# Kernel optimization log

Measured on AMD Instinct MI355X. Metric: run time of the kernel, lower is better.

Reference implementation:

```python
import jax, jax.numpy as jnp
import numpy as np

D_MODEL = 1024
D_HIDDEN = 4096
NUM_EXPERTS = 8
K_ACTIVE = 2


def setup_inputs() -> dict:
    key = jax.random.key(0)
    ks = jax.random.split(key, 8)
    x = jax.random.normal(ks[0], (1, 2048, D_MODEL), dtype=jnp.float32)
    gate_w = jax.random.normal(ks[1], (D_MODEL, NUM_EXPERTS), dtype=jnp.float32) * 0.02
    gate_b = jnp.zeros((NUM_EXPERTS,), dtype=jnp.float32)
    w1 = jax.random.normal(ks[2], (NUM_EXPERTS, D_MODEL, D_HIDDEN), dtype=jnp.float32) * 0.02
    b1 = jnp.zeros((NUM_EXPERTS, D_HIDDEN), dtype=jnp.float32)
    w2 = jax.random.normal(ks[3], (NUM_EXPERTS, D_HIDDEN, D_MODEL), dtype=jnp.float32) * 0.02
    b2 = jnp.zeros((NUM_EXPERTS, D_MODEL), dtype=jnp.float32)
    return {"x": x, "gate_w": gate_w, "gate_b": gate_b,
            "w1": w1, "b1": b1, "w2": w2, "b2": b2}


def reference(x, gate_w, gate_b, w1, b1, w2, b2):
    B, S, D = x.shape
    xf = x.reshape(-1, D)                                    # [T, D]
    logits = xf @ gate_w + gate_b                            # [T, E]
    top_w, top_idx = jax.lax.top_k(logits, K_ACTIVE)         # [T, K]
    top_w = jax.nn.softmax(top_w, axis=-1)                   # softmax over selected experts
    # combine-weight per expert: sum over k slots of one-hot(idx) * weight -> [T, E]
    gates = jnp.sum(jax.nn.one_hot(top_idx, NUM_EXPERTS, dtype=xf.dtype) * top_w[..., None], axis=1)
    # expert FFN applied per expert (dropout is identity in eval): gelu is exact (erf), matching torch nn.GELU default
    h = jax.nn.gelu(jnp.einsum('td,edh->teh', xf, w1) + b1[None], approximate=False)  # [T, E, H]
    y = jnp.einsum('teh,ehd->ted', h, w2) + b2[None]         # [T, E, D]
    out = jnp.einsum('ted,te->td', y, gates)                 # weighted combine of selected experts
    return out.reshape(B, S, D)
```

## Files before the change

### kernel.cpp

```cpp
#include <hip/hip_runtime.h>
#include <stdint.h>

typedef unsigned short u16;
typedef __attribute__((ext_vector_type(8))) short s16x8;
typedef __attribute__((ext_vector_type(8))) u16  u16x8;
typedef __attribute__((ext_vector_type(4))) u16  u16x4;
typedef __attribute__((ext_vector_type(4))) float f32x4;

#define T_TOKENS 2048
#define DM 1024
#define DH 4096
#define NE 8
#define BM 128
#define BN 128
#define BK 64
#define MAXSLOTS (T_TOKENS*2 + NE*BM)
#define ROWBLK (MAXSLOTS/BM)

__device__ __forceinline__ u16 f2bf(float f) {
    union { float ff; uint32_t u; } v; v.ff = f;
    uint32_t r = v.u + 0x7fffu + ((v.u >> 16) & 1u);
    return (u16)(r >> 16);
}

#define GLOAD_LDS16(gsrc, ldst) \
    __builtin_amdgcn_global_load_lds((const __attribute__((address_space(1))) uint32_t*)(gsrc), \
                                     (__attribute__((address_space(3))) uint32_t*)(ldst), 16, 0, 0)

#define WAIT_VM8() asm volatile("s_waitcnt vmcnt(8)" ::: "memory")
#define WAIT_VM0() asm volatile("s_waitcnt vmcnt(0)" ::: "memory")

__global__ void k_convert(const float* __restrict__ x, u16* __restrict__ xbf,
                          int* __restrict__ ctrl) {
    int i = blockIdx.x * blockDim.x + threadIdx.x;
    const f32x4* xv = (const f32x4*)x;
    f32x4 a = xv[2*i], b = xv[2*i+1];
    u16x8 o;
    o[0]=f2bf(a[0]); o[1]=f2bf(a[1]); o[2]=f2bf(a[2]); o[3]=f2bf(a[3]);
    o[4]=f2bf(b[0]); o[5]=f2bf(b[1]); o[6]=f2bf(b[2]); o[7]=f2bf(b[3]);
    ((u16x8*)xbf)[i] = o;
    if (blockIdx.x == 0 && threadIdx.x < 32) ctrl[threadIdx.x] = 0;
}

__global__ void __launch_bounds__(256) k_transpose(const float* __restrict__ src,
                                                   u16* __restrict__ dst,
                                                   int K, int N) {
    __shared__ float tile[64][65];
    const int e = blockIdx.z;
    const int n0 = blockIdx.x * 64, k0 = blockIdx.y * 64;
    const float* s = src + (size_t)e * K * N;
    u16* d = dst + (size_t)e * K * N;
    const int tx = threadIdx.x & 15, ty = threadIdx.x >> 4;
    #pragma unroll
    for (int j = 0; j < 4; ++j) {
        int r = ty * 4 + j;
        f32x4 v = *(const f32x4*)(s + (size_t)(k0 + r) * N + n0 + tx * 4);
        tile[r][tx*4+0] = v[0]; tile[r][tx*4+1] = v[1];
        tile[r][tx*4+2] = v[2]; tile[r][tx*4+3] = v[3];
    }
    __syncthreads();
    #pragma unroll
    for (int j = 0; j < 4; ++j) {
        int n = ty * 4 + j;
        u16x4 w;
        #pragma unroll
        for (int c = 0; c < 4; ++c) w[c] = f2bf(tile[tx*4+c][n]);
        *(u16x4*)(d + (size_t)(n0 + n) * K + k0 + tx * 4) = w;
    }
}

__global__ void __launch_bounds__(64) k_gate(const float* __restrict__ x,
                                             const float* __restrict__ gw,
                                             const float* __restrict__ gb,
                                             int* __restrict__ cnt,
                                             int* __restrict__ tt_idx,
                                             float* __restrict__ tt_w) {
    const int t = blockIdx.x;
    const int lane = threadIdx.x;
    float acc[NE] = {0.f,0.f,0.f,0.f,0.f,0.f,0.f,0.f};
    const float* xr = x + (size_t)t * DM;
    #pragma unroll
    for (int c = 0; c < DM/64; ++c) {
        float xv = xr[lane + 64*c];
        const float* g = gw + (size_t)(lane + 64*c) * NE;
        #pragma unroll
        for (int e = 0; e < NE; ++e) acc[e] += xv * g[e];
    }
    #pragma unroll
    for (int e = 0; e < NE; ++e) {
        #pragma unroll
        for (int off = 32; off >= 1; off >>= 1)
            acc[e] += __shfl_xor(acc[e], off, 64);
    }
    if (lane == 0) {
        float l[NE];
        #pragma unroll
        for (int e = 0; e < NE; ++e) l[e] = acc[e] + gb[e];
        int i0 = 0;
        #pragma unroll
        for (int e = 1; e < NE; ++e) if (l[e] > l[i0]) i0 = e;
        int i1 = (i0 == 0) ? 1 : 0;
        #pragma unroll
        for (int e = 0; e < NE; ++e) if (e != i0 && l[e] > l[i1]) i1 = e;
        float m  = l[i0];
        float w0 = expf(l[i0] - m), w1 = expf(l[i1] - m);
        float s = w0 + w1; w0 /= s; w1 /= s;
        tt_idx[t*2] = i0; tt_idx[t*2+1] = i1;
        tt_w[t*2] = w0;  tt_w[t*2+1] = w1;
        atomicAdd(&cnt[i0], 1); atomicAdd(&cnt[i1], 1);
    }
}

__global__ void k_offsets(const int* __restrict__ cnt, int* __restrict__ fill,
                          int* __restrict__ off) {
    if (threadIdx.x == 0 && blockIdx.x == 0) {
        int a = 0;
        for (int e = 0; e < NE; ++e) {
            off[e] = a;
            a += (cnt[e] + BM - 1) / BM * BM;
            fill[e] = 0;
        }
        off[NE] = a;
    }
}

__global__ void k_scatter(const int* __restrict__ tt_idx, const float* __restrict__ tt_w,
                          const int* __restrict__ off, int* __restrict__ fill,
                          int* __restrict__ slot_token, float* __restrict__ slot_gate,
                          int* __restrict__ tok_slot) {
    int t = blockIdx.x * blockDim.x + threadIdx.x;
    if (t >= T_TOKENS) return;
    #pragma unroll
    for (int k = 0; k < 2; ++k) {
        int e = tt_idx[t*2+k];
        int pos = off[e] + atomicAdd(&fill[e], 1);
        slot_token[pos] = t;
        slot_gate[pos]  = tt_w[t*2+k];
        tok_slot[t*2+k] = pos;
    }
}

__device__ __forceinline__ void mma64(const u16* As, const u16* Bs, int lane,
                                      int wr, int wc, f32x4 acc[4][4]) {
    #pragma unroll
    for (int ko = 0; ko < 2; ++ko) {
        s16x8 af[4], bfr[4];
        #pragma unroll
        for (int m = 0; m < 4; ++m) {
            int row = wr*64 + m*16 + (lane & 15);
            int sl = (ko*4 + (lane >> 4)) ^ (row & 7);
            af[m] = *(const s16x8*)&As[row*BK + sl*8];
        }
        #pragma unroll
        for (int n = 0; n < 4; ++n) {
            int col = wc*64 + n*16 + (lane & 15);
            int sl = (ko*4 + (lane >> 4)) ^ (col & 7);
            bfr[n] = *(const s16x8*)&Bs[col*BK + sl*8];
        }
        #pragma unroll
        for (int m = 0; m < 4; ++m)
            #pragma unroll
            for (int n = 0; n < 4; ++n)
                acc[m][n] = __builtin_amdgcn_mfma_f32_16x16x32_bf16(af[m], bfr[n], acc[m][n], 0, 0, 0);
    }
}


__global__ void __launch_bounds__(256) k_ffn1_b16(
    const u16* __restrict__ xbf, const u16* __restrict__ w1t,
    const float* __restrict__ b1, const int* __restrict__ slot_token,
    const int* __restrict__ off, u16* __restrict__ h)
{
    __shared__ u16 As[2][BM*BK];
    __shared__ u16 Bs[2][BN*BK];
    const int rb = blockIdx.y, cb = blockIdx.x;
    const int total = off[NE];
    const int r0 = rb * BM;
    if (r0 >= total) return;
    int e = 0;
    while (e < NE-1 && off[e+1] <= r0) e++;
    const u16* Bsrc = w1t + (size_t)e * DM * DH;
    const float* be = b1 + (size_t)e * DH;

    const int tid = threadIdx.x;
    const int lane = tid & 63, wid = tid >> 6;
    const int wr = wid >> 1, wc = wid & 1;

    const u16* gA[4]; const u16* gB[4];
    #pragma unroll
    for (int i = 0; i < 4; ++i) {
        int row = wid*32 + i*8 + (lane >> 3);
        int g = (lane & 7) ^ (row & 7);
        int tok = slot_token[r0 + row];
        gA[i] = xbf + (size_t)tok * DM + g*8;
        gB[i] = Bsrc + (size_t)(cb*BN + row) * DM + g*8;
    }

    f32x4 acc[4][4];
    #pragma unroll
    for (int m = 0; m < 4; ++m)
        #pragma unroll
        for (int n = 0; n < 4; ++n) acc[m][n] = (f32x4){0.f,0.f,0.f,0.f};

    #define STAGE1(buf, kt) do {                                              \
        _Pragma("unroll")                                                     \
        for (int i = 0; i < 4; ++i) {                                         \
            GLOAD_LDS16(gA[i] + (kt)*BK, &As[buf][(wid*32 + i*8)*BK]);        \
            GLOAD_LDS16(gB[i] + (kt)*BK, &Bs[buf][(wid*32 + i*8)*BK]);        \
        }                                                                     \
    } while (0)

    const int NT = DM / BK;
    STAGE1(0, 0);
    STAGE1(1, 1);
    #pragma unroll 1
    for (int kt = 0; kt < NT; ++kt) {
        if (kt + 1 < NT) WAIT_VM8(); else WAIT_VM0();
        __builtin_amdgcn_s_barrier();
        __builtin_amdgcn_s_setprio(1);
        mma64(As[kt & 1], Bs[kt & 1], lane, wr, wc, acc);
        __builtin_amdgcn_s_setprio(0);
        __builtin_amdgcn_s_barrier();
        if (kt + 2 < NT) STAGE1(kt & 1, kt + 2);
    }
    #undef STAGE1

    #pragma unroll
    for (int n = 0; n < 4; ++n) {
        int col = cb*BN + wc*64 + n*16 + (lane & 15);
        float bb = be[col];
        #pragma unroll
        for (int m = 0; m < 4; ++m) {
            int rbase = r0 + wr*64 + m*16 + (lane >> 4)*4;
            #pragma unroll
            for (int i = 0; i < 4; ++i) {
                float v = acc[m][n][i] + bb;
                float gv = 0.5f * v * (1.0f + erff(v * 0.70710678118654752f));
                h[(size_t)(rbase + i)*DH + col] = f2bf(gv);
            }
        }
    }
}

__global__ void __launch_bounds__(256) k_ffn2_b16(
    const u16* __restrict__ h, const u16* __restrict__ w2t,
    const float* __restrict__ b2, const int* __restrict__ slot_token,
    const float* __restrict__ slot_gate, const int* __restrict__ off,
    float* __restrict__ out, float* __restrict__ partial, int ktiles)
{
    __shared__ u16 As[2][BM*BK];
    __shared__ u16 Bs[2][BN*BK];
    const int rb = blockIdx.y, cb = blockIdx.x, kz = blockIdx.z;
    const int total = off[NE];
    const int r0 = rb * BM;
    if (r0 >= total) return;
    int e = 0;
    while (e < NE-1 && off[e+1] <= r0) e++;
    const u16* Bsrc = w2t + (size_t)e * DH * DM;
    const float* be = b2 + (size_t)e * DM;
    const int kt0 = kz * ktiles;

    const int tid = threadIdx.x;
    const int lane = tid & 63, wid = tid >> 6;
    const int wr = wid >> 1, wc = wid & 1;

    const u16* gA[4]; const u16* gB[4];
    #pragma unroll
    for (int i = 0; i < 4; ++i) {
        int row = wid*32 + i*8 + (lane >> 3);
        int g = (lane & 7) ^ (row & 7);
        gA[i] = h + (size_t)(r0 + row) * DH + (size_t)kt0*BK + g*8;
        gB[i] = Bsrc + (size_t)(cb*BN + row) * DH + (size_t)kt0*BK + g*8;
    }

    f32x4 acc[4][4];
    #pragma unroll
    for (int m = 0; m < 4; ++m)
        #pragma unroll
        for (int n = 0; n < 4; ++n) acc[m][n] = (f32x4){0.f,0.f,0.f,0.f};

    #define STAGE2(buf, kt) do {                                              \
        _Pragma("unroll")                                                     \
        for (int i = 0; i < 4; ++i) {                                         \
            GLOAD_LDS16(gA[i] + (kt)*BK, &As[buf][(wid*32 + i*8)*BK]);        \
            GLOAD_LDS16(gB[i] + (kt)*BK, &Bs[buf][(wid*32 + i*8)*BK]);        \
        }                                                                     \
    } while (0)

    const int NT = ktiles;
    STAGE2(0, 0);
    STAGE2(1, 1);
    #pragma unroll 1
    for (int kt = 0; kt < NT; ++kt) {
        if (kt + 1 < NT) WAIT_VM8(); else WAIT_VM0();
        __builtin_amdgcn_s_barrier();
        __builtin_amdgcn_s_setprio(1);
        mma64(As[kt & 1], Bs[kt & 1], lane, wr, wc, acc);
        __builtin_amdgcn_s_setprio(0);
        __builtin_amdgcn_s_barrier();
        if (kt + 2 < NT) STAGE2(kt & 1, kt + 2);
    }
    #undef STAGE2

    if (partial) {
        #pragma unroll
        for (int m = 0; m < 4; ++m) {
            #pragma unroll
            for (int i = 0; i < 4; ++i) {
                int s = r0 + wr*64 + m*16 + (lane >> 4)*4 + i;
                float* prow = partial + (size_t)s * DM + cb*BN + wc*64;
                #pragma unroll
                for (int n = 0; n < 4; ++n)
                    atomicAdd(prow + n*16 + (lane & 15), acc[m][n][i]);
            }
        }
    } else {
        float bb[4];
        #pragma unroll
        for (int n = 0; n < 4; ++n) bb[n] = be[cb*BN + wc*64 + n*16 + (lane & 15)];
        #pragma unroll
        for (int m = 0; m < 4; ++m) {
            #pragma unroll
            for (int i = 0; i < 4; ++i) {
                int s = r0 + wr*64 + m*16 + (lane >> 4)*4 + i;
                int tok = slot_token[s];
                float g = slot_gate[s];
                if (g != 0.0f) {
                    float* orow = out + (size_t)tok * DM + cb*BN + wc*64;
                    #pragma unroll
                    for (int n = 0; n < 4; ++n)
                        atomicAdd(orow + n*16 + (lane & 15), g * (acc[m][n][i] + bb[n]));
                }
            }
        }
    }
}

__global__ void __launch_bounds__(256) k_combine(
    const float* __restrict__ partial, const float* __restrict__ b2,
    const int* __restrict__ tok_slot, const int* __restrict__ tt_idx,
    const float* __restrict__ tt_w, float* __restrict__ out)
{
    const int t = blockIdx.x;
    const int d = threadIdx.x * 4;
    const int s0 = tok_slot[t*2], s1 = tok_slot[t*2+1];
    const int e0 = tt_idx[t*2],  e1 = tt_idx[t*2+1];
    const float g0 = tt_w[t*2],  g1 = tt_w[t*2+1];
    f32x4 p0 = *(const f32x4*)(partial + (size_t)s0 * DM + d);
    f32x4 p1 = *(const f32x4*)(partial + (size_t)s1 * DM + d);
    f32x4 bb0 = *(const f32x4*)(b2 + (size_t)e0 * DM + d);
    f32x4 bb1 = *(const f32x4*)(b2 + (size_t)e1 * DM + d);
    f32x4 o;
    #pragma unroll
    for (int c = 0; c < 4; ++c) o[c] = g0 * (p0[c] + bb0[c]) + g1 * (p1[c] + bb1[c]);
    *(f32x4*)(out + (size_t)t * DM + d) = o;
}


__global__ void __launch_bounds__(256) k_ffn1_f32(
    const u16* __restrict__ xbf, const float* __restrict__ w1,
    const float* __restrict__ b1, const int* __restrict__ slot_token,
    const int* __restrict__ off, u16* __restrict__ h)
{
    __shared__ u16 As[BM*BK];
    __shared__ u16 Bs[BN*BK];
    const int rb = blockIdx.y, cb = blockIdx.x;
    const int total = off[NE];
    const int r0 = rb * BM;
    if (r0 >= total) return;
    int e = 0;
    while (e < NE-1 && off[e+1] <= r0) e++;
    const float* Bsrc = w1 + (size_t)e * DM * DH;
    const float* be   = b1 + (size_t)e * DH;

    const int tid = threadIdx.x;
    const int lane = tid & 63, wid = tid >> 6;
    const int wr = wid >> 1, wc = wid & 1;

    const u16* gA[4];
    #pragma unroll
    for (int i = 0; i < 4; ++i) {
        int row = wid*32 + i*8 + (lane >> 3);
        int g = (lane & 7) ^ (row & 7);
        int tok = slot_token[r0 + row];
        gA[i] = xbf + (size_t)tok * DM + g*8;
    }
    const int tc = tid & 31, tr = tid >> 5;
    const float* gB = Bsrc + (size_t)(tr*8) * DH + cb*BN + tc*4;

    f32x4 acc[4][4];
    #pragma unroll
    for (int m = 0; m < 4; ++m)
        #pragma unroll
        for (int n = 0; n < 4; ++n) acc[m][n] = (f32x4){0.f,0.f,0.f,0.f};

    for (int kt = 0; kt < DM/BK; ++kt) {
        #pragma unroll
        for (int i = 0; i < 4; ++i)
            GLOAD_LDS16(gA[i] + kt*BK, &As[(wid*32 + i*8)*BK]);
        f32x4 bv[8];
        #pragma unroll
        for (int j = 0; j < 8; ++j)
            bv[j] = *(const f32x4*)(gB + (size_t)(kt*BK + j) * DH);
        #pragma unroll
        for (int c = 0; c < 4; ++c) {
            int n = tc*4 + c;
            int sl = tr ^ (n & 7);
            s16x8 pk;
            #pragma unroll
            for (int j = 0; j < 8; ++j) pk[j] = (short)f2bf(bv[j][c]);
            *(s16x8*)&Bs[n*BK + sl*8] = pk;
        }
        __syncthreads();
        mma64(As, Bs, lane, wr, wc, acc);
        __syncthreads();
    }
    #pragma unroll
    for (int n = 0; n < 4; ++n) {
        int col = cb*BN + wc*64 + n*16 + (lane & 15);
        float bb = be[col];
        #pragma unroll
        for (int m = 0; m < 4; ++m) {
            int rbase = r0 + wr*64 + m*16 + (lane >> 4)*4;
            #pragma unroll
            for (int i = 0; i < 4; ++i) {
                float v = acc[m][n][i] + bb;
                float gv = 0.5f * v * (1.0f + erff(v * 0.70710678118654752f));
                h[(size_t)(rbase + i)*DH + col] = f2bf(gv);
            }
        }
    }
}

__global__ void __launch_bounds__(256) k_ffn2_f32(
    const u16* __restrict__ h, const float* __restrict__ w2,
    const float* __restrict__ b2, const int* __restrict__ slot_token,
    const float* __restrict__ slot_gate, const int* __restrict__ off,
    float* __restrict__ out)
{
    __shared__ u16 As[BM*BK];
    __shared__ u16 Bs[BN*BK];
    const int rb = blockIdx.y, cb = blockIdx.x;
    const int total = off[NE];
    const int r0 = rb * BM;
    if (r0 >= total) return;
    int e = 0;
    while (e < NE-1 && off[e+1] <= r0) e++;
    const float* Bsrc = w2 + (size_t)e * DH * DM;
    const float* be   = b2 + (size_t)e * DM;

    const int tid = threadIdx.x;
    const int lane = tid & 63, wid = tid >> 6;
    const int wr = wid >> 1, wc = wid & 1;

    const u16* gA[4];
    #pragma unroll
    for (int i = 0; i < 4; ++i) {
        int row = wid*32 + i*8 + (lane >> 3);
        int g = (lane & 7) ^ (row & 7);
        gA[i] = h + (size_t)(r0 + row) * DH + g*8;
    }
    const int tc = tid & 31, tr = tid >> 5;
    const float* gB = Bsrc + (size_t)(tr*8) * DM + cb*BN + tc*4;

    f32x4 acc[4][4];
    #pragma unroll
    for (int m = 0; m < 4; ++m)
        #pragma unroll
        for (int n = 0; n < 4; ++n) acc[m][n] = (f32x4){0.f,0.f,0.f,0.f};

    for (int kt = 0; kt < DH/BK; ++kt) {
        #pragma unroll
        for (int i = 0; i < 4; ++i)
            GLOAD_LDS16(gA[i] + kt*BK, &As[(wid*32 + i*8)*BK]);
        f32x4 bv[8];
        #pragma unroll
        for (int j = 0; j < 8; ++j)
            bv[j] = *(const f32x4*)(gB + (size_t)(kt*BK + j) * DM);
        #pragma unroll
        for (int c = 0; c < 4; ++c) {
            int n = tc*4 + c;
            int sl = tr ^ (n & 7);
            s16x8 pk;
            #pragma unroll
            for (int j = 0; j < 8; ++j) pk[j] = (short)f2bf(bv[j][c]);
            *(s16x8*)&Bs[n*BK + sl*8] = pk;
        }
        __syncthreads();
        mma64(As, Bs, lane, wr, wc, acc);
        __syncthreads();
    }
    float bb[4];
    #pragma unroll
    for (int n = 0; n < 4; ++n) bb[n] = be[cb*BN + wc*64 + n*16 + (lane & 15)];
    #pragma unroll
    for (int m = 0; m < 4; ++m) {
        #pragma unroll
        for (int i = 0; i < 4; ++i) {
            int s = r0 + wr*64 + m*16 + (lane >> 4)*4 + i;
            int tok = slot_token[s];
            float g = slot_gate[s];
            if (g != 0.0f) {
                float* orow = out + (size_t)tok * DM + cb*BN + wc*64;
                #pragma unroll
                for (int n = 0; n < 4; ++n)
                    atomicAdd(orow + n*16 + (lane & 15), g * (acc[m][n][i] + bb[n]));
            }
        }
    }
}

extern "C" void kernel_launch(void* const* d_in, const int* in_sizes, int n_in,
                              void* d_out, int out_size, void* d_ws, size_t ws_size,
                              hipStream_t stream)
{
    (void)in_sizes; (void)n_in; (void)out_size;
    const float* x  = (const float*)d_in[0];
    const float* gw = (const float*)d_in[1];
    const float* gb = (const float*)d_in[2];
    const float* w1 = (const float*)d_in[3];
    const float* b1 = (const float*)d_in[4];
    const float* w2 = (const float*)d_in[5];
    const float* b2 = (const float*)d_in[6];
    float* out = (float*)d_out;
    char* ws = (char*)d_ws;

    const size_t OFF_XBF = 0;
    const size_t OFF_H   = 4194304;
    const size_t OFF_WT  = OFF_H + (size_t)MAXSLOTS * DH * 2;
    const size_t OFF_ST  = OFF_WT + (size_t)NE * DM * DH * 2;
    const size_t OFF_SG  = OFF_ST + MAXSLOTS * 4;
    const size_t OFF_TI  = OFF_SG + MAXSLOTS * 4;
    const size_t OFF_TW  = OFF_TI + T_TOKENS * 2 * 4;
    const size_t OFF_TS  = OFF_TW + T_TOKENS * 2 * 4;
    const size_t OFF_CT  = OFF_TS + T_TOKENS * 2 * 4;
    const size_t NEED_B16 = OFF_CT + 128;
    const size_t OFF_PT  = (NEED_B16 + 255) & ~(size_t)255;
    const size_t NEED_SPLIT = OFF_PT + (size_t)MAXSLOTS * DM * 4;

    if (ws_size >= NEED_B16) {
        u16*   xbf        = (u16*)(ws + OFF_XBF);
        u16*   h          = (u16*)(ws + OFF_H);
        u16*   wt         = (u16*)(ws + OFF_WT);
        int*   slot_token = (int*)(ws + OFF_ST);
        float* slot_gate  = (float*)(ws + OFF_SG);
        int*   tt_idx     = (int*)(ws + OFF_TI);
        float* tt_w       = (float*)(ws + OFF_TW);
        int*   tok_slot   = (int*)(ws + OFF_TS);
        int*   ctrl       = (int*)(ws + OFF_CT);
        float* partial    = (float*)(ws + OFF_PT);
        int* cnt = ctrl; int* fill = ctrl + 8; int* offs = ctrl + 16;
        const int use_split = (ws_size >= NEED_SPLIT);

        hipMemsetAsync(slot_token, 0, 2 * MAXSLOTS * 4, stream);
        if (use_split)
            hipMemsetAsync(partial, 0, (size_t)MAXSLOTS * DM * 4, stream);
        else
            hipMemsetAsync(out, 0, (size_t)T_TOKENS * DM * sizeof(float), stream);

        k_convert<<<(T_TOKENS*DM/8 + 255)/256, 256, 0, stream>>>(x, xbf, ctrl);
        k_gate<<<T_TOKENS, 64, 0, stream>>>(x, gw, gb, cnt, tt_idx, tt_w);
        k_offsets<<<1, 64, 0, stream>>>(cnt, fill, offs);
        k_scatter<<<(T_TOKENS + 255)/256, 256, 0, stream>>>(tt_idx, tt_w, offs, fill,
                                                            slot_token, slot_gate, tok_slot);

        k_transpose<<<dim3(DH/64, DM/64, NE), 256, 0, stream>>>(w1, wt, DM, DH);
        k_ffn1_b16<<<dim3(DH/BN, ROWBLK), 256, 0, stream>>>(xbf, wt, b1, slot_token, offs, h);
        k_transpose<<<dim3(DM/64, DH/64, NE), 256, 0, stream>>>(w2, wt, DH, DM);

        if (use_split) {
            k_ffn2_b16<<<dim3(DM/BN, ROWBLK, 2), 256, 0, stream>>>(
                h, wt, b2, slot_token, slot_gate, offs, out, partial, DH/BK/2);
            k_combine<<<T_TOKENS, 256, 0, stream>>>(partial, b2, tok_slot, tt_idx, tt_w, out);
        } else {
            k_ffn2_b16<<<dim3(DM/BN, ROWBLK, 1), 256, 0, stream>>>(
                h, wt, b2, slot_token, slot_gate, offs, out, (float*)nullptr, DH/BK);
        }
    } else {
        u16*   xbf        = (u16*)(ws);
        u16*   h          = (u16*)(ws + 4194304);
        int*   slot_token = (int*)(ws + 46137344);
        float* slot_gate  = (float*)(ws + 46157824);
        int*   tt_idx     = (int*)(ws + 46178304);
        float* tt_w       = (float*)(ws + 46194688);
        int*   tok_slot   = (int*)(ws + 46211072);
        int*   ctrl       = (int*)(ws + 46227456);
        int* cnt = ctrl; int* fill = ctrl + 8; int* offs = ctrl + 16;

        hipMemsetAsync(slot_token, 0, 2 * MAXSLOTS * 4, stream);
        hipMemsetAsync(out, 0, (size_t)T_TOKENS * DM * sizeof(float), stream);

        k_convert<<<(T_TOKENS*DM/8 + 255)/256, 256, 0, stream>>>(x, xbf, ctrl);
        k_gate<<<T_TOKENS, 64, 0, stream>>>(x, gw, gb, cnt, tt_idx, tt_w);
        k_offsets<<<1, 64, 0, stream>>>(cnt, fill, offs);
        k_scatter<<<(T_TOKENS + 255)/256, 256, 0, stream>>>(tt_idx, tt_w, offs, fill,
                                                            slot_token, slot_gate, tok_slot);
        k_ffn1_f32<<<dim3(DH/BN, ROWBLK), 256, 0, stream>>>(xbf, w1, b1, slot_token, offs, h);
        k_ffn2_f32<<<dim3(DM/BN, ROWBLK), 256, 0, stream>>>(h, w2, b2, slot_token, slot_gate, offs, out);
    }
}
```

Baseline: 341.3 us.

## Use 256x256 tiles for FFN1, pad experts to 256, drop FFN2 split-K

Replaces the 128x128 first-layer expert GEMM with a 256x256-tile kernel using 512 threads and 8x4 MFMA accumulators per wave, and pads each expert's slot range to 256 rows. The larger tile raises data reuse per LDS load and halves the number of row blocks. The split-K second GEMM with its partial buffer and combine pass is removed, so FFN2 always atomically adds gated results straight into the output. A half-width weight transpose path is added for smaller workspaces. The extra padding rows add wasted compute, and the larger tile raises register and LDS pressure.

```diff
diff --git a/kernel.cpp b/kernel.cpp
--- a/kernel.cpp
+++ b/kernel.cpp
@@ -11,9 +11,13 @@
 #define DM 1024
 #define DH 4096
 #define NE 8
+#define BK 64
+#define PAD2 256
+#define MAXS2 (T_TOKENS*2 + NE*PAD2)
+#define RB1 (MAXS2/256)
+#define RB2 (MAXS2/128)
 #define BM 128
 #define BN 128
-#define BK 64
 #define MAXSLOTS (T_TOKENS*2 + NE*BM)
 #define ROWBLK (MAXSLOTS/BM)
 
@@ -44,12 +48,12 @@
 
 __global__ void __launch_bounds__(256) k_transpose(const float* __restrict__ src,
                                                    u16* __restrict__ dst,
-                                                   int K, int N) {
+                                                   int K, int N, int nw0, int NW) {
     __shared__ float tile[64][65];
     const int e = blockIdx.z;
-    const int n0 = blockIdx.x * 64, k0 = blockIdx.y * 64;
+    const int n0 = nw0 + blockIdx.x * 64, k0 = blockIdx.y * 64;
     const float* s = src + (size_t)e * K * N;
-    u16* d = dst + (size_t)e * K * N;
+    u16* d = dst + (size_t)e * K * NW;
     const int tx = threadIdx.x & 15, ty = threadIdx.x >> 4;
     #pragma unroll
     for (int j = 0; j < 4; ++j) {
@@ -65,7 +69,7 @@
         u16x4 w;
         #pragma unroll
         for (int c = 0; c < 4; ++c) w[c] = f2bf(tile[tx*4+c][n]);
-        *(u16x4*)(d + (size_t)(n0 + n) * K + k0 + tx * 4) = w;
+        *(u16x4*)(d + (size_t)(n0 - nw0 + n) * K + k0 + tx * 4) = w;
     }
 }
 
@@ -112,12 +116,12 @@
 }
 
 __global__ void k_offsets(const int* __restrict__ cnt, int* __restrict__ fill,
-                          int* __restrict__ off) {
+                          int* __restrict__ off, int pad) {
     if (threadIdx.x == 0 && blockIdx.x == 0) {
         int a = 0;
         for (int e = 0; e < NE; ++e) {
             off[e] = a;
-            a += (cnt[e] + BM - 1) / BM * BM;
+            a += (cnt[e] + pad - 1) / pad * pad;
             fill[e] = 0;
         }
         off[NE] = a;
@@ -126,8 +130,7 @@
 
 __global__ void k_scatter(const int* __restrict__ tt_idx, const float* __restrict__ tt_w,
                           const int* __restrict__ off, int* __restrict__ fill,
-                          int* __restrict__ slot_token, float* __restrict__ slot_gate,
-                          int* __restrict__ tok_slot) {
+                          int* __restrict__ slot_token, float* __restrict__ slot_gate) {
     int t = blockIdx.x * blockDim.x + threadIdx.x;
     if (t >= T_TOKENS) return;
     #pragma unroll
@@ -136,7 +139,6 @@
         int pos = off[e] + atomicAdd(&fill[e], 1);
         slot_token[pos] = t;
         slot_gate[pos]  = tt_w[t*2+k];
-        tok_slot[t*2+k] = pos;
     }
 }
 
@@ -165,11 +167,113 @@
     }
 }
 
-
-__global__ void __launch_bounds__(256) k_ffn1_b16(
-    const u16* __restrict__ xbf, const u16* __restrict__ w1t,
+__device__ __forceinline__ void mma256(const u16* As, const u16* Bs, int lane,
+                                       int wr, int wc, f32x4 acc[8][4]) {
+    #pragma unroll
+    for (int ko = 0; ko < 2; ++ko) {
+        s16x8 af[8], bfr[4];
+        #pragma unroll
+        for (int m = 0; m < 8; ++m) {
+            int row = wr*128 + m*16 + (lane & 15);
+            int sl = (ko*4 + (lane >> 4)) ^ (row & 7);
+            af[m] = *(const s16x8*)&As[row*BK + sl*8];
+        }
+        #pragma unroll
+        for (int n = 0; n < 4; ++n) {
+            int col = wc*64 + n*16 + (lane & 15);
+            int sl = (ko*4 + (lane >> 4)) ^ (col & 7);
+            bfr[n] = *(const s16x8*)&Bs[col*BK + sl*8];
+        }
+        #pragma unroll
+        for (int m = 0; m < 8; ++m)
+            #pragma unroll
+            for (int n = 0; n < 4; ++n)
+                acc[m][n] = __builtin_amdgcn_mfma_f32_16x16x32_bf16(af[m], bfr[n], acc[m][n], 0, 0, 0);
+    }
+}
+
+__global__ void __launch_bounds__(512, 2) k_ffn1_256(
+    const u16* __restrict__ xbf, const u16* __restrict__ wt,
     const float* __restrict__ b1, const int* __restrict__ slot_token,
-    const int* __restrict__ off, u16* __restrict__ h)
+    const int* __restrict__ off, u16* __restrict__ h, int cb0, int NW)
+{
+    __shared__ u16 As[2][256*BK];
+    __shared__ u16 Bs[2][256*BK];
+    const int rb = blockIdx.y, cbl = blockIdx.x;
+    const int total = off[NE];
+    const int r0 = rb * 256;
+    if (r0 >= total) return;
+    int e = 0;
+    while (e < NE-1 && off[e+1] <= r0) e++;
+    const u16* Bsrc = wt + (size_t)e * DM * NW;
+    const float* be = b1 + (size_t)e * DH;
+    const int colbase = (cb0 + cbl) * 256;
+
+    const int tid = threadIdx.x;
+    const int lane = tid & 63, wid = tid >> 6;
+    const int wr = wid >> 2, wc = wid & 3;
+
+    const u16* gA[4]; const u16* gB[4];
+    #pragma unroll
+    for (int i = 0; i < 4; ++i) {
+        int row = wid*32 + i*8 + (lane >> 3);
+        int g = (lane & 7) ^ (row & 7);
+        int tok = slot_token[r0 + row];
+        gA[i] = xbf + (size_t)tok * DM + g*8;
+        gB[i] = Bsrc + (size_t)(cbl*256 + row) * DM + g*8;
+    }
+
+    f32x4 acc[8][4];
+    #pragma unroll
+    for (int m = 0; m < 8; ++m)
+        #pragma unroll
+        for (int n = 0; n < 4; ++n) acc[m][n] = (f32x4){0.f,0.f,0.f,0.f};
+
+    #define STG1(buf, kt) do {                                                \
+        _Pragma("unroll")                                                     \
+        for (int i = 0; i < 4; ++i) {                                         \
+            GLOAD_LDS16(gA[i] + (kt)*BK, &As[buf][(wid*32 + i*8)*BK]);        \
+            GLOAD_LDS16(gB[i] + (kt)*BK, &Bs[buf][(wid*32 + i*8)*BK]);        \
+        }                                                                     \
+    } while (0)
+
+    const int NT = DM / BK;
+    STG1(0, 0);
+    STG1(1, 1);
+    #pragma unroll 1
+    for (int kt = 0; kt < NT; ++kt) {
+        if (kt + 1 < NT) WAIT_VM8(); else WAIT_VM0();
+        __builtin_amdgcn_s_barrier();
+        __builtin_amdgcn_s_setprio(1);
+        mma256(As[kt & 1], Bs[kt & 1], lane, wr, wc, acc);
+        __builtin_amdgcn_s_setprio(0);
+        __builtin_amdgcn_s_barrier();
+        if (kt + 2 < NT) STG1(kt & 1, kt + 2);
+    }
+    #undef STG1
+
+    #pragma unroll
+    for (int n = 0; n < 4; ++n) {
+        int col = colbase + wc*64 + n*16 + (lane & 15);
+        float bb = be[col];
+        #pragma unroll
+        for (int m = 0; m < 8; ++m) {
+            int rbase = r0 + wr*128 + m*16 + (lane >> 4)*4;
+            #pragma unroll
+            for (int i = 0; i < 4; ++i) {
+                float v = acc[m][n][i] + bb;
+                float gv = 0.5f * v * (1.0f + erff(v * 0.70710678118654752f));
+                h[(size_t)(rbase + i)*DH + col] = f2bf(gv);
+            }
+        }
+    }
+}
+
+__global__ void __launch_bounds__(256) k_ffn2_b16(
+    const u16* __restrict__ h, const u16* __restrict__ w2t,
+    const float* __restrict__ b2, const int* __restrict__ slot_token,
+    const float* __restrict__ slot_gate, const int* __restrict__ off,
+    float* __restrict__ out)
 {
     __shared__ u16 As[2][BM*BK];
     __shared__ u16 Bs[2][BN*BK];
@@ -179,8 +283,8 @@
     if (r0 >= total) return;
     int e = 0;
     while (e < NE-1 && off[e+1] <= r0) e++;
-    const u16* Bsrc = w1t + (size_t)e * DM * DH;
-    const float* be = b1 + (size_t)e * DH;
+    const u16* Bsrc = w2t + (size_t)e * DH * DM;
+    const float* be = b2 + (size_t)e * DM;
 
     const int tid = threadIdx.x;
     const int lane = tid & 63, wid = tid >> 6;
@@ -191,9 +295,8 @@
     for (int i = 0; i < 4; ++i) {
         int row = wid*32 + i*8 + (lane >> 3);
         int g = (lane & 7) ^ (row & 7);
-        int tok = slot_token[r0 + row];
-        gA[i] = xbf + (size_t)tok * DM + g*8;
-        gB[i] = Bsrc + (size_t)(cb*BN + row) * DM + g*8;
+        gA[i] = h + (size_t)(r0 + row) * DH + g*8;
+        gB[i] = Bsrc + (size_t)(cb*BN + row) * DH + g*8;
     }
 
     f32x4 acc[4][4];
@@ -202,7 +305,7 @@
         #pragma unroll
         for (int n = 0; n < 4; ++n) acc[m][n] = (f32x4){0.f,0.f,0.f,0.f};
 
-    #define STAGE1(buf, kt) do {                                              \
+    #define STG2(buf, kt) do {                                                \
         _Pragma("unroll")                                                     \
         for (int i = 0; i < 4; ++i) {                                         \
             GLOAD_LDS16(gA[i] + (kt)*BK, &As[buf][(wid*32 + i*8)*BK]);        \
@@ -210,9 +313,9 @@
         }                                                                     \
     } while (0)
 
-    const int NT = DM / BK;
-    STAGE1(0, 0);
-    STAGE1(1, 1);
+    const int NT = DH / BK;
+    STG2(0, 0);
+    STG2(1, 1);
     #pragma unroll 1
     for (int kt = 0; kt < NT; ++kt) {
         if (kt + 1 < NT) WAIT_VM8(); else WAIT_VM0();
@@ -221,139 +324,28 @@
         mma64(As[kt & 1], Bs[kt & 1], lane, wr, wc, acc);
         __builtin_amdgcn_s_setprio(0);
         __builtin_amdgcn_s_barrier();
-        if (kt + 2 < NT) STAGE1(kt & 1, kt + 2);
-    }
-    #undef STAGE1
-
-    #pragma unroll
-    for (int n = 0; n < 4; ++n) {
-        int col = cb*BN + wc*64 + n*16 + (lane & 15);
-        float bb = be[col];
-        #pragma unroll
-        for (int m = 0; m < 4; ++m) {
-            int rbase = r0 + wr*64 + m*16 + (lane >> 4)*4;
-            #pragma unroll
-            for (int i = 0; i < 4; ++i) {
-                float v = acc[m][n][i] + bb;
-                float gv = 0.5f * v * (1.0f + erff(v * 0.70710678118654752f));
-                h[(size_t)(rbase + i)*DH + col] = f2bf(gv);
-            }
-        }
-    }
-}
-
-__global__ void __launch_bounds__(256) k_ffn2_b16(
-    const u16* __restrict__ h, const u16* __restrict__ w2t,
-    const float* __restrict__ b2, const int* __restrict__ slot_token,
-    const float* __restrict__ slot_gate, const int* __restrict__ off,
-    float* __restrict__ out, float* __restrict__ partial, int ktiles)
-{
-    __shared__ u16 As[2][BM*BK];
-    __shared__ u16 Bs[2][BN*BK];
-    const int rb = blockIdx.y, cb = blockIdx.x, kz = blockIdx.z;
-    const int total = off[NE];
-    const int r0 = rb * BM;
-    if (r0 >= total) return;
-    int e = 0;
-    while (e < NE-1 && off[e+1] <= r0) e++;
-    const u16* Bsrc = w2t + (size_t)e * DH * DM;
-    const float* be = b2 + (size_t)e * DM;
-    const int kt0 = kz * ktiles;
-
-    const int tid = threadIdx.x;
-    const int lane = tid & 63, wid = tid >> 6;
-    const int wr = wid >> 1, wc = wid & 1;
-
-    const u16* gA[4]; const u16* gB[4];
-    #pragma unroll
-    for (int i = 0; i < 4; ++i) {
-        int row = wid*32 + i*8 + (lane >> 3);
-        int g = (lane & 7) ^ (row & 7);
-        gA[i] = h + (size_t)(r0 + row) * DH + (size_t)kt0*BK + g*8;
-        gB[i] = Bsrc + (size_t)(cb*BN + row) * DH + (size_t)kt0*BK + g*8;
-    }
-
-    f32x4 acc[4][4];
-    #pragma unroll
-    for (int m = 0; m < 4; ++m)
-        #pragma unroll
-        for (int n = 0; n < 4; ++n) acc[m][n] = (f32x4){0.f,0.f,0.f,0.f};
-
-    #define STAGE2(buf, kt) do {                                              \
-        _Pragma("unroll")                                                     \
-        for (int i = 0; i < 4; ++i) {                                         \
-            GLOAD_LDS16(gA[i] + (kt)*BK, &As[buf][(wid*32 + i*8)*BK]);        \
-            GLOAD_LDS16(gB[i] + (kt)*BK, &Bs[buf][(wid*32 + i*8)*BK]);        \
-        }                                                                     \
-    } while (0)
-
-    const int NT = ktiles;
-    STAGE2(0, 0);
-    STAGE2(1, 1);
-    #pragma unroll 1
-    for (int kt = 0; kt < NT; ++kt) {
-        if (kt + 1 < NT) WAIT_VM8(); else WAIT_VM0();
-        __builtin_amdgcn_s_barrier();
-        __builtin_amdgcn_s_setprio(1);
-        mma64(As[kt & 1], Bs[kt & 1], lane, wr, wc, acc);
-        __builtin_amdgcn_s_setprio(0);
-        __builtin_amdgcn_s_barrier();
-        if (kt + 2 < NT) STAGE2(kt & 1, kt + 2);
-    }
-    #undef STAGE2
-
-    if (partial) {
-        #pragma unroll
-        for (int m = 0; m < 4; ++m) {
-            #pragma unroll
-            for (int i = 0; i < 4; ++i) {
-                int s = r0 + wr*64 + m*16 + (lane >> 4)*4 + i;
-                float* prow = partial + (size_t)s * DM + cb*BN + wc*64;
+        if (kt + 2 < NT) STG2(kt & 1, kt + 2);
+    }
+    #undef STG2
+
+    float bb[4];
+    #pragma unroll
+    for (int n = 0; n < 4; ++n) bb[n] = be[cb*BN + wc*64 + n*16 + (lane & 15)];
+    #pragma unroll
+    for (int m = 0; m < 4; ++m) {
+        #pragma unroll
+        for (int i = 0; i < 4; ++i) {
+            int s = r0 + wr*64 + m*16 + (lane >> 4)*4 + i;
+            int tok = slot_token[s];
+            float g = slot_gate[s];
+            if (g != 0.0f) {
+                float* orow = out + (size_t)tok * DM + cb*BN + wc*64;
                 #pragma unroll
                 for (int n = 0; n < 4; ++n)
-                    atomicAdd(prow + n*16 + (lane & 15), acc[m][n][i]);
+                    atomicAdd(orow + n*16 + (lane & 15), g * (acc[m][n][i] + bb[n]));
             }
         }
-    } else {
-        float bb[4];
-        #pragma unroll
-        for (int n = 0; n < 4; ++n) bb[n] = be[cb*BN + wc*64 + n*16 + (lane & 15)];
-        #pragma unroll
-        for (int m = 0; m < 4; ++m) {
-            #pragma unroll
-            for (int i = 0; i < 4; ++i) {
-                int s = r0 + wr*64 + m*16 + (lane >> 4)*4 + i;
-                int tok = slot_token[s];
-                float g = slot_gate[s];
-                if (g != 0.0f) {
-                    float* orow = out + (size_t)tok * DM + cb*BN + wc*64;
-                    #pragma unroll
-                    for (int n = 0; n < 4; ++n)
-                        atomicAdd(orow + n*16 + (lane & 15), g * (acc[m][n][i] + bb[n]));
-                }
-            }
-        }
-    }
-}
-
-__global__ void __launch_bounds__(256) k_combine(
-    const float* __restrict__ partial, const float* __restrict__ b2,
-    const int* __restrict__ tok_slot, const int* __restrict__ tt_idx,
-    const float* __restrict__ tt_w, float* __restrict__ out)
-{
-    const int t = blockIdx.x;
-    const int d = threadIdx.x * 4;
-    const int s0 = tok_slot[t*2], s1 = tok_slot[t*2+1];
-    const int e0 = tt_idx[t*2],  e1 = tt_idx[t*2+1];
-    const float g0 = tt_w[t*2],  g1 = tt_w[t*2+1];
-    f32x4 p0 = *(const f32x4*)(partial + (size_t)s0 * DM + d);
-    f32x4 p1 = *(const f32x4*)(partial + (size_t)s1 * DM + d);
-    f32x4 bb0 = *(const f32x4*)(b2 + (size_t)e0 * DM + d);
-    f32x4 bb1 = *(const f32x4*)(b2 + (size_t)e1 * DM + d);
-    f32x4 o;
-    #pragma unroll
-    for (int c = 0; c < 4; ++c) o[c] = g0 * (p0[c] + bb0[c]) + g1 * (p1[c] + bb1[c]);
-    *(f32x4*)(out + (size_t)t * DM + d) = o;
+    }
 }
 
 
@@ -527,55 +519,46 @@
 
     const size_t OFF_XBF = 0;
     const size_t OFF_H   = 4194304;
-    const size_t OFF_WT  = OFF_H + (size_t)MAXSLOTS * DH * 2;
-    const size_t OFF_ST  = OFF_WT + (size_t)NE * DM * DH * 2;
-    const size_t OFF_SG  = OFF_ST + MAXSLOTS * 4;
-    const size_t OFF_TI  = OFF_SG + MAXSLOTS * 4;
+    const size_t OFF_ST  = OFF_H + (size_t)MAXS2 * DH * 2;
+    const size_t OFF_SG  = OFF_ST + MAXS2 * 4;
+    const size_t OFF_TI  = OFF_SG + MAXS2 * 4;
     const size_t OFF_TW  = OFF_TI + T_TOKENS * 2 * 4;
-    const size_t OFF_TS  = OFF_TW + T_TOKENS * 2 * 4;
-    const size_t OFF_CT  = OFF_TS + T_TOKENS * 2 * 4;
-    const size_t NEED_B16 = OFF_CT + 128;
-    const size_t OFF_PT  = (NEED_B16 + 255) & ~(size_t)255;
-    const size_t NEED_SPLIT = OFF_PT + (size_t)MAXSLOTS * DM * 4;
-
-    if (ws_size >= NEED_B16) {
+    const size_t OFF_CT  = OFF_TW + T_TOKENS * 2 * 4;
+    const size_t OFF_WT  = (OFF_CT + 128 + 255) & ~(size_t)255;
+    const size_t NEED_FULL = OFF_WT + (size_t)NE * DM * DH * 2;
+    const size_t NEED_HALF = OFF_WT + (size_t)NE * DM * (DH/2) * 2;
+
+    if (ws_size >= NEED_HALF) {
         u16*   xbf        = (u16*)(ws + OFF_XBF);
         u16*   h          = (u16*)(ws + OFF_H);
-        u16*   wt         = (u16*)(ws + OFF_WT);
         int*   slot_token = (int*)(ws + OFF_ST);
         float* slot_gate  = (float*)(ws + OFF_SG);
         int*   tt_idx     = (int*)(ws + OFF_TI);
         float* tt_w       = (float*)(ws + OFF_TW);
-        int*   tok_slot   = (int*)(ws + OFF_TS);
         int*   ctrl       = (int*)(ws + OFF_CT);
-        float* partial    = (float*)(ws + OFF_PT);
+        u16*   wt         = (u16*)(ws + OFF_WT);
         int* cnt = ctrl; int* fill = ctrl + 8; int* offs = ctrl + 16;
-        const int use_split = (ws_size >= NEED_SPLIT);
-
-        hipMemsetAsync(slot_token, 0, 2 * MAXSLOTS * 4, stream);
-        if (use_split)
-            hipMemsetAsync(partial, 0, (size_t)MAXSLOTS * DM * 4, stream);
-        else
-            hipMemsetAsync(out, 0, (size_t)T_TOKENS * DM * sizeof(float), stream);
+        const int full = (ws_size >= NEED_FULL);
+
+        hipMemsetAsync(slot_token, 0, 2 * MAXS2 * 4, stream);
+        hipMemsetAsync(out, 0, (size_t)T_TOKENS * DM * sizeof(float), stream);
 
         k_convert<<<(T_TOKENS*DM/8 + 255)/256, 256, 0, stream>>>(x, xbf, ctrl);
         k_gate<<<T_TOKENS, 64, 0, stream>>>(x, gw, gb, cnt, tt_idx, tt_w);
-        k_offsets<<<1, 64, 0, stream>>>(cnt, fill, offs);
+        k_offsets<<<1, 64, 0, stream>>>(cnt, fill, offs, PAD2);
         k_scatter<<<(T_TOKENS + 255)/256, 256, 0, stream>>>(tt_idx, tt_w, offs, fill,
-                                                            slot_token, slot_gate, tok_slot);
-
-        k_transpose<<<dim3(DH/64, DM/64, NE), 256, 0, stream>>>(w1, wt, DM, DH);
-        k_ffn1_b16<<<dim3(DH/BN, ROWBLK), 256, 0, stream>>>(xbf, wt, b1, slot_token, offs, h);
-        k_transpose<<<dim3(DM/64, DH/64, NE), 256, 0, stream>>>(w2, wt, DH, DM);
-
-        if (use_split) {
-            k_ffn2_b16<<<dim3(DM/BN, ROWBLK, 2), 256, 0, stream>>>(
-                h, wt, b2, slot_token, slot_gate, offs, out, partial, DH/BK/2);
-            k_combine<<<T_TOKENS, 256, 0, stream>>>(partial, b2, tok_slot, tt_idx, tt_w, out);
+                                                            slot_token, slot_gate);
+        if (full) {
+            k_transpose<<<dim3(DH/64, DM/64, NE), 256, 0, stream>>>(w1, wt, DM, DH, 0, DH);
+            k_ffn1_256<<<dim3(DH/256, RB1), 512, 0, stream>>>(xbf, wt, b1, slot_token, offs, h, 0, DH);
         } else {
-            k_ffn2_b16<<<dim3(DM/BN, ROWBLK, 1), 256, 0, stream>>>(
-                h, wt, b2, slot_token, slot_gate, offs, out, (float*)nullptr, DH/BK);
-        }
+            k_transpose<<<dim3(DH/128, DM/64, NE), 256, 0, stream>>>(w1, wt, DM, DH, 0, DH/2);
+            k_ffn1_256<<<dim3(DH/512, RB1), 512, 0, stream>>>(xbf, wt, b1, slot_token, offs, h, 0, DH/2);
+            k_transpose<<<dim3(DH/128, DM/64, NE), 256, 0, stream>>>(w1, wt, DM, DH, DH/2, DH/2);
+            k_ffn1_256<<<dim3(DH/512, RB1), 512, 0, stream>>>(xbf, wt, b1, slot_token, offs, h, DH/512, DH/2);
+        }
+        k_transpose<<<dim3(DM/64, DH/64, NE), 256, 0, stream>>>(w2, wt, DH, DM, 0, DM);
+        k_ffn2_b16<<<dim3(DM/BN, RB2), 256, 0, stream>>>(h, wt, b2, slot_token, slot_gate, offs, out);
     } else {
         u16*   xbf        = (u16*)(ws);
         u16*   h          = (u16*)(ws + 4194304);
@@ -583,8 +566,7 @@
         float* slot_gate  = (float*)(ws + 46157824);
         int*   tt_idx     = (int*)(ws + 46178304);
         float* tt_w       = (float*)(ws + 46194688);
-        int*   tok_slot   = (int*)(ws + 46211072);
-        int*   ctrl       = (int*)(ws + 46227456);
+        int*   ctrl       = (int*)(ws + 46211072);
         int* cnt = ctrl; int* fill = ctrl + 8; int* offs = ctrl + 16;
 
         hipMemsetAsync(slot_token, 0, 2 * MAXSLOTS * 4, stream);
@@ -592,9 +574,9 @@
 
         k_convert<<<(T_TOKENS*DM/8 + 255)/256, 256, 0, stream>>>(x, xbf, ctrl);
         k_gate<<<T_TOKENS, 64, 0, stream>>>(x, gw, gb, cnt, tt_idx, tt_w);
-        k_offsets<<<1, 64, 0, stream>>>(cnt, fill, offs);
+        k_offsets<<<1, 64, 0, stream>>>(cnt, fill, offs, BM);
         k_scatter<<<(T_TOKENS + 255)/256, 256, 0, stream>>>(tt_idx, tt_w, offs, fill,
-                                                            slot_token, slot_gate, tok_slot);
+                                                            slot_token, slot_gate);
         k_ffn1_f32<<<dim3(DH/BN, ROWBLK), 256, 0, stream>>>(xbf, w1, b1, slot_token, offs, h);
         k_ffn2_f32<<<dim3(DM/BN, ROWBLK), 256, 0, stream>>>(h, w2, b2, slot_token, slot_gate, offs, out);
     }
```

Measured after the change: 343.5 us. About the same (+0.7%).
